# Optimization experiments

Hardware: AMD Instinct MI355X
Metric: run time of the kernel (lower is better)

Reference implementation:

```python
import jax, jax.numpy as jnp
import numpy as np

B, T, DIN, DM, NC = 8, 4096, 1024, 256, 157
DILS = (1, 2, 4, 8, 16)


def _conv1(w, x, b=None):
    # 1x1 conv: w [out,in], x [B,in,T] -> [B,out,T]
    y = jnp.einsum('oi,bit->bot', w, x)
    return y if b is None else y + b[None, :, None]


def _dal(x, wq, wk, wv, d):
    # Dilated 3-tap multiplicative local attention (DAL block, groups=1).
    # Taps in the zero-padded (pad=d) sequence at offsets 0, d, 2d == positions t-d, t, t+d.
    _, _, T_ = x.shape
    xp = jnp.pad(x, ((0, 0), (0, 0), (d, d)))
    q = _conv1(wq, x)                 # [B,C,T]
    kp = _conv1(wk, xp)               # [B,C,T+2d]
    vp = _conv1(wv, xp)
    k = jnp.stack([kp[:, :, 0:T_], kp[:, :, d:T_ + d], kp[:, :, 2 * d:T_ + 2 * d]], axis=-1)  # [B,C,T,3]
    v = jnp.stack([vp[:, :, 0:T_], vp[:, :, d:T_ + d], vp[:, :, 2 * d:T_ + 2 * d]], axis=-1)
    attn = jax.nn.softmax(q[..., None] * k, axis=-1)  # softmax over the 3 taps
    return jnp.sum(attn * v, axis=-1)  # [B,C,T]


def _fwd(x, mask, bottle0_w, bottle0_b,
         dal1_wq, dal1_wk, dal1_wv, bottle1_w, bottle1_b,
         dal2_wq, dal2_wk, dal2_wv, bottle2_w, bottle2_b,
         dal3_wq, dal3_wk, dal3_wv, bottle3_w, bottle3_b,
         dal4_wq, dal4_wk, dal4_wv, bottle4_w, bottle4_b,
         dal5_wq, dal5_wk, dal5_wv, bottle5_w, bottle5_b,
         bottle6_w, bottle6_b):
    m = mask[:, 0:1, :]
    out = _conv1(bottle0_w, x, bottle0_b)
    layers = [
        (dal1_wq, dal1_wk, dal1_wv, bottle1_w, bottle1_b),
        (dal2_wq, dal2_wk, dal2_wv, bottle2_w, bottle2_b),
        (dal3_wq, dal3_wk, dal3_wv, bottle3_w, bottle3_b),
        (dal4_wq, dal4_wk, dal4_wv, bottle4_w, bottle4_b),
        (dal5_wq, dal5_wk, dal5_wv, bottle5_w, bottle5_b),
    ]
    # Dropout layers are identity in eval mode.
    for (wq, wk, wv, bw, bb), d in zip(layers, DILS):
        h = jax.nn.relu(_dal(out, wq, wk, wv, d))
        h = _conv1(bw, h, bb)
        out = (out + h) * m
    return _conv1(bottle6_w, out, bottle6_b) * m  # [B,NC,T]


def setup_inputs() -> dict:
    key = jax.random.key(0)
    ks = jax.random.split(key, 32)
    s = 0.05
    inp = {}
    inp['x'] = jax.random.normal(ks[0], (B, DIN, T), jnp.float32)
    inp['mask'] = jnp.ones((B, 1, T), jnp.float32)
    inp['bottle0_w'] = jax.random.normal(ks[1], (DM, DIN), jnp.float32) * s
    inp['bottle0_b'] = jnp.zeros((DM,), jnp.float32)
    i = 2
    for l in range(1, 6):
        inp['dal%d_wq' % l] = jax.random.normal(ks[i], (DM, DM), jnp.float32) * s; i += 1
        inp['dal%d_wk' % l] = jax.random.normal(ks[i], (DM, DM), jnp.float32) * s; i += 1
        inp['dal%d_wv' % l] = jax.random.normal(ks[i], (DM, DM), jnp.float32) * s; i += 1
        inp['bottle%d_w' % l] = jax.random.normal(ks[i], (DM, DM), jnp.float32) * s; i += 1
        inp['bottle%d_b' % l] = jnp.zeros((DM,), jnp.float32)
    inp['bottle6_w'] = jax.random.normal(ks[i], (NC, DM), jnp.float32) * s
    inp['bottle6_b'] = jnp.zeros((NC,), jnp.float32)
    return inp


def reference(x, mask, bottle0_w, bottle0_b,
              dal1_wq, dal1_wk, dal1_wv, bottle1_w, bottle1_b,
              dal2_wq, dal2_wk, dal2_wv, bottle2_w, bottle2_b,
              dal3_wq, dal3_wk, dal3_wv, bottle3_w, bottle3_b,
              dal4_wq, dal4_wk, dal4_wv, bottle4_w, bottle4_b,
              dal5_wq, dal5_wk, dal5_wv, bottle5_w, bottle5_b,
              bottle6_w, bottle6_b):
    return _fwd(x, mask, bottle0_w, bottle0_b,
                dal1_wq, dal1_wk, dal1_wv, bottle1_w, bottle1_b,
                dal2_wq, dal2_wk, dal2_wv, bottle2_w, bottle2_b,
                dal3_wq, dal3_wk, dal3_wv, bottle3_w, bottle3_b,
                dal4_wq, dal4_wk, dal4_wv, bottle4_w, bottle4_b,
                dal5_wq, dal5_wk, dal5_wv, bottle5_w, bottle5_b,
                bottle6_w, bottle6_b)
```

## Files before the change

### kernel.cpp

```cpp
#include <hip/hip_runtime.h>
#include <hip/hip_bf16.h>
#include <stdint.h>

#define T_LEN 4096
#define B_SZ  8
#define D_IN  1024
#define D_M   256
#define N_C   157

typedef __attribute__((ext_vector_type(8))) short short8;
typedef __attribute__((ext_vector_type(4))) float floatx4;

static __device__ __forceinline__ unsigned short f2bf(float f) {
  unsigned u = __float_as_uint(f);
  u += 0x7FFFu + ((u >> 16) & 1u);
  return (unsigned short)(u >> 16);
}
static __device__ __forceinline__ float bf2f(unsigned short h) {
  return __uint_as_float(((unsigned)h) << 16);
}

static __device__ __forceinline__ void gl_lds16(const unsigned short* g,
                                                unsigned short* l) {
  __builtin_amdgcn_global_load_lds(
      (const __attribute__((address_space(1))) unsigned int*)g,
      (__attribute__((address_space(3))) unsigned int*)l, 16, 0, 0);
}

struct WSeg { const float* src; int n; int off; };
struct WPrepArgs { WSeg seg[22]; };

__global__ void wprep_kernel(WPrepArgs a, unsigned short* __restrict__ wbuf) {
  WSeg s = a.seg[blockIdx.x];
  for (int i = (blockIdx.y << 8) + threadIdx.x; i < s.n; i += (gridDim.y << 8))
    wbuf[s.off + i] = f2bf(s.src[i]);
}

__global__ void transpose_xT(const float* __restrict__ x,
                             unsigned short* __restrict__ xT) {
  __shared__ float tile[64][65];
  const int t0 = blockIdx.x << 6;
  const int i0 = blockIdx.y << 6;
  const int b  = blockIdx.z;
  const int tid = threadIdx.x;
  {
    const int row = tid >> 2;
    const int cc  = (tid & 3) << 4;
    const float* src = x + ((size_t)b * D_IN + (i0 + row)) * T_LEN + t0 + cc;
#pragma unroll
    for (int p = 0; p < 4; ++p) {
      float4 v = *(const float4*)(src + p * 4);
      tile[row][cc + p * 4 + 0] = v.x;
      tile[row][cc + p * 4 + 1] = v.y;
      tile[row][cc + p * 4 + 2] = v.z;
      tile[row][cc + p * 4 + 3] = v.w;
    }
  }
  __syncthreads();
#pragma unroll
  for (int it = 0; it < 2; ++it) {
    const int task = tid + (it << 8);
    const int tr = task >> 3;
    const int ic = (task & 7) << 3;
    short8 o;
#pragma unroll
    for (int j = 0; j < 8; ++j) o[j] = (short)f2bf(tile[ic + j][tr]);
    *(short8*)(xT + ((size_t)b * T_LEN + (t0 + tr)) * D_IN + i0 + ic) = o;
  }
}

template<bool ATTN, bool HAS_BIAS, bool HAS_RES, bool HAS_MASK,
         bool WRITE_BF16, bool SWAP_CT>
__global__ __launch_bounds__(256)
void gemm_kernel(const unsigned short* __restrict__ Xact,
                 const unsigned short* __restrict__ W,
                 const float* __restrict__ bias,
                 const unsigned short* __restrict__ residB,
                 const float* __restrict__ mask,
                 float* __restrict__ outF,
                 unsigned short* __restrict__ outB,
                 int K, int Mw, int dil) {
  __shared__ unsigned short sA[2][64 * 64];
  __shared__ unsigned short sB[2][128 * 64];

  const int bx = blockIdx.x;
  const int t0 = blockIdx.y << (SWAP_CT ? 7 : 6);
  const int b  = blockIdx.z;
  const int tid  = threadIdx.x;
  const int wv   = tid >> 6;
  const int lane = tid & 63;
  const int wn   = wv << 5;
  const int fm   = lane & 15;
  const int fq   = lane >> 4;
  const int lrow = lane >> 3;
  const int cbg8 = (((lane & 7) ^ lrow) << 3);

  const unsigned short* Xb =
      Xact + (size_t)b * T_LEN * (size_t)(ATTN ? 768 : K);
  const unsigned short* srcA =
      SWAP_CT ? (W + (size_t)(bx << 6) * K) : (Xb + (size_t)t0 * K);
  const unsigned short* srcB =
      SWAP_CT ? (Xb + (size_t)t0 * K) : (W + (size_t)(bx << 7) * K);

  const short8 z8 = {0, 0, 0, 0, 0, 0, 0, 0};
  const floatx4 fz = {0.f, 0.f, 0.f, 0.f};
  floatx4 acc[4][2];
#pragma unroll
  for (int i = 0; i < 4; ++i)
#pragma unroll
    for (int j = 0; j < 2; ++j) acc[i][j] = fz;

  auto stage = [&](int kk, int bufi) {
    if constexpr (ATTN) {
#pragma unroll
      for (int itp = 0; itp < 2; ++itp) {
        int c = tid + (itp << 8);
        int m = c >> 3;
        int cb = c & 7;
        int ch = kk + (cb << 3);
        int t = t0 + m;
        const unsigned short* base = Xb + (size_t)t * 768 + ch;
        short8 qv = *(const short8*)(base);
        short8 kc = *(const short8*)(base + 256);
        short8 vc = *(const short8*)(base + 512);
        short8 km = z8, kp = z8, vm = z8, vp = z8;
        const long off = (long)dil * 768;
        if (t >= dil) {
          km = *(const short8*)(base - off + 256);
          vm = *(const short8*)(base - off + 512);
        }
        if (t + dil < T_LEN) {
          kp = *(const short8*)(base + off + 256);
          vp = *(const short8*)(base + off + 512);
        }
        short8 o;
#pragma unroll
        for (int e = 0; e < 8; ++e) {
          float q  = bf2f((unsigned short)qv[e]);
          float s0 = q * bf2f((unsigned short)km[e]);
          float s1 = q * bf2f((unsigned short)kc[e]);
          float s2 = q * bf2f((unsigned short)kp[e]);
          float mx = fmaxf(s0, fmaxf(s1, s2));
          float e0 = __expf(s0 - mx), e1 = __expf(s1 - mx), e2 = __expf(s2 - mx);
          float num = e0 * bf2f((unsigned short)vm[e]) +
                      e1 * bf2f((unsigned short)vc[e]) +
                      e2 * bf2f((unsigned short)vp[e]);
          float r = num / (e0 + e1 + e2);
          o[e] = (short)f2bf(fmaxf(r, 0.0f));
        }
        *(short8*)&sA[bufi][(m << 6) + ((cb ^ (m & 7)) << 3)] = o;
      }
    } else {
#pragma unroll
      for (int p = 0; p < 2; ++p) {
        const int slot = (p << 2) + wv;
        gl_lds16(srcA + (size_t)((slot << 3) + lrow) * K + kk + cbg8,
                 &sA[bufi][slot * 512]);
      }
    }
#pragma unroll
    for (int p = 0; p < 4; ++p) {
      const int slot = (p << 2) + wv;
      gl_lds16(srcB + (size_t)((slot << 3) + lrow) * K + kk + cbg8,
               &sB[bufi][slot * 512]);
    }
  };

  const int niter = K >> 6;
  stage(0, 0);
  for (int it = 0; it < niter; ++it) {
    const int p = it & 1;
    __syncthreads();
    if (it + 1 < niter) stage((it + 1) << 6, 1 - p);
#pragma unroll
    for (int ks = 0; ks < 64; ks += 32) {
      const int cbase = ((fq + (ks >> 3)) ^ (fm & 7)) << 3;
      short8 af[4], bfr[2];
#pragma unroll
      for (int i = 0; i < 4; ++i)
        af[i] = *(short8*)&sA[p][(((i << 4) + fm) << 6) + cbase];
#pragma unroll
      for (int j = 0; j < 2; ++j)
        bfr[j] = *(short8*)&sB[p][((wn + (j << 4) + fm) << 6) + cbase];
#pragma unroll
      for (int i = 0; i < 4; ++i)
#pragma unroll
        for (int j = 0; j < 2; ++j)
          acc[i][j] = __builtin_amdgcn_mfma_f32_16x16x32_bf16(
              af[i], bfr[j], acc[i][j], 0, 0, 0);
    }
  }

  if constexpr (SWAP_CT) {
#pragma unroll
    for (int i = 0; i < 4; ++i) {
#pragma unroll
      for (int r = 0; r < 4; ++r) {
        const int o = (bx << 6) + (i << 4) + (fq << 2) + r;
        if (o >= Mw) continue;
        const float bi = HAS_BIAS ? bias[o] : 0.0f;
#pragma unroll
        for (int j = 0; j < 2; ++j) {
          const int t = t0 + wn + (j << 4) + fm;
          float val = acc[i][j][r] + bi;
          if (HAS_MASK) val *= mask[(size_t)b * T_LEN + t];
          outF[((size_t)b * Mw + o) * T_LEN + t] = val;
        }
      }
    }
  } else {
#pragma unroll
    for (int i = 0; i < 4; ++i) {
#pragma unroll
      for (int j = 0; j < 2; ++j) {
        const int co = (bx << 7) + wn + (j << 4) + fm;
        if (co >= Mw) continue;
        const float bi = HAS_BIAS ? bias[co] : 0.0f;
#pragma unroll
        for (int r = 0; r < 4; ++r) {
          const int t = t0 + (i << 4) + (fq << 2) + r;
          float val = acc[i][j][r] + bi;
          const size_t idx = ((size_t)b * T_LEN + t) * (size_t)Mw + co;
          if (HAS_RES) val += bf2f(residB[idx]);
          if (HAS_MASK) val *= mask[(size_t)b * T_LEN + t];
          if (WRITE_BF16) outB[idx] = f2bf(val);
        }
      }
    }
  }
}

extern "C" void kernel_launch(void* const* d_in, const int* in_sizes, int n_in,
                              void* d_out, int out_size, void* d_ws, size_t ws_size,
                              hipStream_t stream) {
  const float* x    = (const float*)d_in[0];
  const float* mask = (const float*)d_in[1];

  char* ws = (char*)d_ws;
  unsigned short* xT   = (unsigned short*)ws;
  unsigned short* qkv  = xT;
  unsigned short* outB = (unsigned short*)(ws + 67108864);
  unsigned short* wbuf = (unsigned short*)(ws + 83886080);

  const int WB0  = 0;
  const int WQKV = 262144;
  const int WBT  = 1245184;
  const int WB6  = 1572864;

  WPrepArgs pa;
  int si = 0;
  pa.seg[si++] = { (const float*)d_in[2], 262144, WB0 };
  for (int l = 0; l < 5; ++l) {
    int bi = 4 + l * 5;
    pa.seg[si++] = { (const float*)d_in[bi + 0], 65536, WQKV + l * 196608 };
    pa.seg[si++] = { (const float*)d_in[bi + 1], 65536, WQKV + l * 196608 + 65536 };
    pa.seg[si++] = { (const float*)d_in[bi + 2], 65536, WQKV + l * 196608 + 131072 };
    pa.seg[si++] = { (const float*)d_in[bi + 3], 65536, WBT + l * 65536 };
  }
  pa.seg[si++] = { (const float*)d_in[29], 40192, WB6 };

  wprep_kernel<<<dim3(22, 64), 256, 0, stream>>>(pa, wbuf);
  transpose_xT<<<dim3(64, 16, 8), 256, 0, stream>>>(x, xT);

  gemm_kernel<false, true, false, false, true, false>
      <<<dim3(2, 64, 8), 256, 0, stream>>>(
          xT, wbuf + WB0, (const float*)d_in[3], nullptr, mask,
          nullptr, outB, 1024, 256, 0);

  const int dils[5] = {1, 2, 4, 8, 16};
  for (int l = 0; l < 5; ++l) {
    int bi = 4 + l * 5;
    gemm_kernel<false, false, false, false, true, false>
        <<<dim3(6, 64, 8), 256, 0, stream>>>(
            outB, wbuf + WQKV + l * 196608, nullptr, nullptr, mask,
            nullptr, qkv, 256, 768, 0);
    gemm_kernel<true, true, true, true, true, false>
        <<<dim3(2, 64, 8), 256, 0, stream>>>(
            qkv, wbuf + WBT + l * 65536, (const float*)d_in[bi + 4], outB, mask,
            nullptr, outB, 256, 256, dils[l]);
  }

  gemm_kernel<false, true, false, true, false, true>
      <<<dim3(3, 32, 8), 256, 0, stream>>>(
          outB, wbuf + WB6, (const float*)d_in[30], nullptr, mask,
          (float*)d_out, nullptr, 256, 157, 0);
}
```

Before: 653.5 us.

## Fuse QKV projection, dilated attention and bottleneck GEMM into one layer kernel

Result: no change. 660.7 us (+1.1%).

```diff
diff --git a/kernel.cpp b/kernel.cpp
--- a/kernel.cpp
+++ b/kernel.cpp
@@ -69,17 +69,15 @@
   }
 }
 
-template<bool ATTN, bool HAS_BIAS, bool HAS_RES, bool HAS_MASK,
-         bool WRITE_BF16, bool SWAP_CT>
+template<bool HAS_BIAS, bool HAS_MASK, bool SWAP_CT>
 __global__ __launch_bounds__(256)
 void gemm_kernel(const unsigned short* __restrict__ Xact,
                  const unsigned short* __restrict__ W,
                  const float* __restrict__ bias,
-                 const unsigned short* __restrict__ residB,
                  const float* __restrict__ mask,
                  float* __restrict__ outF,
                  unsigned short* __restrict__ outB,
-                 int K, int Mw, int dil) {
+                 int K, int Mw) {
   __shared__ unsigned short sA[2][64 * 64];
   __shared__ unsigned short sB[2][128 * 64];
 
@@ -95,14 +93,12 @@
   const int lrow = lane >> 3;
   const int cbg8 = (((lane & 7) ^ lrow) << 3);
 
-  const unsigned short* Xb =
-      Xact + (size_t)b * T_LEN * (size_t)(ATTN ? 768 : K);
+  const unsigned short* Xb = Xact + (size_t)b * T_LEN * (size_t)K;
   const unsigned short* srcA =
       SWAP_CT ? (W + (size_t)(bx << 6) * K) : (Xb + (size_t)t0 * K);
   const unsigned short* srcB =
       SWAP_CT ? (Xb + (size_t)t0 * K) : (W + (size_t)(bx << 7) * K);
 
-  const short8 z8 = {0, 0, 0, 0, 0, 0, 0, 0};
   const floatx4 fz = {0.f, 0.f, 0.f, 0.f};
   floatx4 acc[4][2];
 #pragma unroll
@@ -111,52 +107,11 @@
     for (int j = 0; j < 2; ++j) acc[i][j] = fz;
 
   auto stage = [&](int kk, int bufi) {
-    if constexpr (ATTN) {
-#pragma unroll
-      for (int itp = 0; itp < 2; ++itp) {
-        int c = tid + (itp << 8);
-        int m = c >> 3;
-        int cb = c & 7;
-        int ch = kk + (cb << 3);
-        int t = t0 + m;
-        const unsigned short* base = Xb + (size_t)t * 768 + ch;
-        short8 qv = *(const short8*)(base);
-        short8 kc = *(const short8*)(base + 256);
-        short8 vc = *(const short8*)(base + 512);
-        short8 km = z8, kp = z8, vm = z8, vp = z8;
-        const long off = (long)dil * 768;
-        if (t >= dil) {
-          km = *(const short8*)(base - off + 256);
-          vm = *(const short8*)(base - off + 512);
-        }
-        if (t + dil < T_LEN) {
-          kp = *(const short8*)(base + off + 256);
-          vp = *(const short8*)(base + off + 512);
-        }
-        short8 o;
-#pragma unroll
-        for (int e = 0; e < 8; ++e) {
-          float q  = bf2f((unsigned short)qv[e]);
-          float s0 = q * bf2f((unsigned short)km[e]);
-          float s1 = q * bf2f((unsigned short)kc[e]);
-          float s2 = q * bf2f((unsigned short)kp[e]);
-          float mx = fmaxf(s0, fmaxf(s1, s2));
-          float e0 = __expf(s0 - mx), e1 = __expf(s1 - mx), e2 = __expf(s2 - mx);
-          float num = e0 * bf2f((unsigned short)vm[e]) +
-                      e1 * bf2f((unsigned short)vc[e]) +
-                      e2 * bf2f((unsigned short)vp[e]);
-          float r = num / (e0 + e1 + e2);
-          o[e] = (short)f2bf(fmaxf(r, 0.0f));
-        }
-        *(short8*)&sA[bufi][(m << 6) + ((cb ^ (m & 7)) << 3)] = o;
-      }
-    } else {
-#pragma unroll
-      for (int p = 0; p < 2; ++p) {
-        const int slot = (p << 2) + wv;
-        gl_lds16(srcA + (size_t)((slot << 3) + lrow) * K + kk + cbg8,
-                 &sA[bufi][slot * 512]);
-      }
+#pragma unroll
+    for (int p = 0; p < 2; ++p) {
+      const int slot = (p << 2) + wv;
+      gl_lds16(srcA + (size_t)((slot << 3) + lrow) * K + kk + cbg8,
+               &sA[bufi][slot * 512]);
     }
 #pragma unroll
     for (int p = 0; p < 4; ++p) {
@@ -220,14 +175,220 @@
         for (int r = 0; r < 4; ++r) {
           const int t = t0 + (i << 4) + (fq << 2) + r;
           float val = acc[i][j][r] + bi;
-          const size_t idx = ((size_t)b * T_LEN + t) * (size_t)Mw + co;
-          if (HAS_RES) val += bf2f(residB[idx]);
           if (HAS_MASK) val *= mask[(size_t)b * T_LEN + t];
-          if (WRITE_BF16) outB[idx] = f2bf(val);
+          outB[((size_t)b * T_LEN + t) * (size_t)Mw + co] = f2bf(val);
         }
       }
     }
   }
+}
+
+__global__ __launch_bounds__(256)
+void layer_kernel(const unsigned short* __restrict__ outPrev,
+                  const unsigned short* __restrict__ Wall,
+                  const unsigned short* __restrict__ Wb,
+                  const float* __restrict__ bias,
+                  const float* __restrict__ mask,
+                  unsigned short* __restrict__ outNext,
+                  int dil) {
+  __shared__ unsigned short lds[70400];
+  unsigned short* xh    = lds;
+  unsigned short* hbuf  = lds + 24576;
+  unsigned short* chunk = lds + 41472;
+  unsigned short* wst   = lds + 62208;
+
+  const int t0 = blockIdx.x << 6;
+  const int b  = blockIdx.y;
+  const int tid  = threadIdx.x;
+  const int wv   = tid >> 6;
+  const int lane = tid & 63;
+  const int fm   = lane & 15;
+  const int fq   = lane >> 4;
+  const int wh   = wv >> 1;
+  const int nh   = wv & 1;
+
+  const unsigned short* src = outPrev + (size_t)b * T_LEN * 256;
+
+#pragma unroll
+  for (int p = 0; p < 12; ++p) {
+    const int slot = (p << 2) + wv;
+    const int row  = (slot << 1) + (lane >> 5);
+    int t = t0 - 16 + row;
+    t = t < 0 ? 0 : (t >= T_LEN ? T_LEN - 1 : t);
+    const int kb = (lane & 31) ^ (row & 7);
+    gl_lds16(src + (size_t)t * 256 + (kb << 3), xh + (slot << 9));
+  }
+  __syncthreads();
+  if (t0 == 0) {
+    *(short8*)&xh[tid << 4] = short8{0,0,0,0,0,0,0,0};
+    *(short8*)&xh[(tid << 4) + 8] = short8{0,0,0,0,0,0,0,0};
+  }
+  if (t0 == T_LEN - 64) {
+    *(short8*)&xh[20480 + (tid << 4)] = short8{0,0,0,0,0,0,0,0};
+    *(short8*)&xh[20480 + (tid << 4) + 8] = short8{0,0,0,0,0,0,0,0};
+  }
+  __syncthreads();
+
+#pragma unroll 1
+  for (int j = 0; j < 4; ++j) {
+#pragma unroll 1
+    for (int sec = 0; sec < 3; ++sec) {
+      const unsigned short* Wsec = Wall + (size_t)((sec << 8) + (j << 6)) * 256;
+#pragma unroll
+      for (int p = 0; p < 2; ++p) {
+        const int slot = (p << 2) + wv;
+        const int rw = (slot << 3) + (lane >> 3);
+        const int kb = (lane & 7) ^ (lane >> 3);
+        gl_lds16(Wsec + (size_t)rw * 256 + (kb << 3), wst + (slot << 9));
+      }
+      floatx4 accB[3][2];
+#pragma unroll
+      for (int i = 0; i < 3; ++i)
+#pragma unroll
+        for (int jj = 0; jj < 2; ++jj) accB[i][jj] = floatx4{0.f,0.f,0.f,0.f};
+
+      for (int kt = 0; kt < 4; ++kt) {
+        __syncthreads();
+        if (kt < 3) {
+          const int nb = (kt + 1) & 1;
+#pragma unroll
+          for (int p = 0; p < 2; ++p) {
+            const int slot = (p << 2) + wv;
+            const int rw = (slot << 3) + (lane >> 3);
+            const int kb = (lane & 7) ^ (lane >> 3);
+            gl_lds16(Wsec + (size_t)rw * 256 + ((kt + 1) << 6) + (kb << 3),
+                     wst + (nb << 12) + (slot << 9));
+          }
+        }
+        const unsigned short* wb = wst + ((kt & 1) << 12);
+#pragma unroll
+        for (int ks = 0; ks < 64; ks += 32) {
+          short8 af[3], bfr[2];
+#pragma unroll
+          for (int i = 0; i < 3; ++i) {
+            const int row = 48 * wh + (i << 4) + fm;
+            const int cb = ((kt << 3) + (ks >> 3) + fq) ^ (fm & 7);
+            af[i] = *(short8*)&xh[(row << 8) + (cb << 3)];
+          }
+#pragma unroll
+          for (int jj = 0; jj < 2; ++jj) {
+            const int nr = (nh << 5) + (jj << 4) + fm;
+            const int cb = ((ks >> 3) + fq) ^ (fm & 7);
+            bfr[jj] = *(short8*)&wb[(nr << 6) + (cb << 3)];
+          }
+#pragma unroll
+          for (int i = 0; i < 3; ++i)
+#pragma unroll
+            for (int jj = 0; jj < 2; ++jj)
+              accB[i][jj] = __builtin_amdgcn_mfma_f32_16x16x32_bf16(
+                  af[i], bfr[jj], accB[i][jj], 0, 0, 0);
+        }
+      }
+#pragma unroll
+      for (int i = 0; i < 3; ++i)
+#pragma unroll
+        for (int jj = 0; jj < 2; ++jj)
+#pragma unroll
+          for (int r = 0; r < 4; ++r) {
+            const int row = 48 * wh + (i << 4) + (fq << 2) + r;
+            const int col = (nh << 5) + (jj << 4) + fm;
+            chunk[sec * 6912 + row * 72 + col] = f2bf(accB[i][jj][r]);
+          }
+    }
+    __syncthreads();
+#pragma unroll
+    for (int p = 0; p < 2; ++p) {
+      const int task = (p << 8) + tid;
+      const int tr = task >> 3;
+      const int c8 = (task & 7) << 3;
+      const int rq = (16 + tr) * 72 + c8;
+      short8 qv = *(short8*)&chunk[rq];
+      short8 kc = *(short8*)&chunk[6912 + rq];
+      short8 vc = *(short8*)&chunk[13824 + rq];
+      short8 km = *(short8*)&chunk[6912 + (16 + tr - dil) * 72 + c8];
+      short8 kp = *(short8*)&chunk[6912 + (16 + tr + dil) * 72 + c8];
+      short8 vm = *(short8*)&chunk[13824 + (16 + tr - dil) * 72 + c8];
+      short8 vp = *(short8*)&chunk[13824 + (16 + tr + dil) * 72 + c8];
+      short8 o;
+#pragma unroll
+      for (int e = 0; e < 8; ++e) {
+        float q  = bf2f((unsigned short)qv[e]);
+        float s0 = q * bf2f((unsigned short)km[e]);
+        float s1 = q * bf2f((unsigned short)kc[e]);
+        float s2 = q * bf2f((unsigned short)kp[e]);
+        float mx = fmaxf(s0, fmaxf(s1, s2));
+        float e0 = __expf(s0 - mx), e1 = __expf(s1 - mx), e2 = __expf(s2 - mx);
+        float num = e0 * bf2f((unsigned short)vm[e]) +
+                    e1 * bf2f((unsigned short)vc[e]) +
+                    e2 * bf2f((unsigned short)vp[e]);
+        float r = num / (e0 + e1 + e2);
+        o[e] = (short)f2bf(fmaxf(r, 0.0f));
+      }
+      *(short8*)&hbuf[tr * 264 + (j << 6) + c8] = o;
+    }
+    __syncthreads();
+  }
+
+  floatx4 accC[4][4];
+#pragma unroll
+  for (int i = 0; i < 4; ++i)
+#pragma unroll
+    for (int jj = 0; jj < 4; ++jj) accC[i][jj] = floatx4{0.f,0.f,0.f,0.f};
+
+#pragma unroll
+  for (int p = 0; p < 4; ++p) {
+    const int slot = (p << 2) + wv;
+    const int rw = (slot << 4) + (lane >> 2);
+    gl_lds16(Wb + (size_t)rw * 256 + ((lane & 3) << 3), chunk + (slot << 9));
+  }
+  for (int kt = 0; kt < 8; ++kt) {
+    __syncthreads();
+    if (kt < 7) {
+      const int nb = (kt + 1) & 1;
+#pragma unroll
+      for (int p = 0; p < 4; ++p) {
+        const int slot = (p << 2) + wv;
+        const int rw = (slot << 4) + (lane >> 2);
+        gl_lds16(Wb + (size_t)rw * 256 + ((kt + 1) << 5) + ((lane & 3) << 3),
+                 chunk + (nb << 13) + (slot << 9));
+      }
+    }
+    const unsigned short* cbuf = chunk + ((kt & 1) << 13);
+    short8 af[4], bfr[4];
+#pragma unroll
+    for (int i = 0; i < 4; ++i) {
+      const int row = (i << 4) + fm;
+      af[i] = *(short8*)&hbuf[row * 264 + (kt << 5) + (fq << 3)];
+    }
+#pragma unroll
+    for (int jj = 0; jj < 4; ++jj) {
+      const int nr = (wv << 6) + (jj << 4) + fm;
+      bfr[jj] = *(short8*)&cbuf[(nr << 5) + (fq << 3)];
+    }
+#pragma unroll
+    for (int i = 0; i < 4; ++i)
+#pragma unroll
+      for (int jj = 0; jj < 4; ++jj)
+        accC[i][jj] = __builtin_amdgcn_mfma_f32_16x16x32_bf16(
+            af[i], bfr[jj], accC[i][jj], 0, 0, 0);
+  }
+
+#pragma unroll
+  for (int i = 0; i < 4; ++i)
+#pragma unroll
+    for (int jj = 0; jj < 4; ++jj) {
+      const int co = (wv << 6) + (jj << 4) + fm;
+      const float bi = bias[co];
+#pragma unroll
+      for (int r = 0; r < 4; ++r) {
+        const int tl = (i << 4) + (fq << 2) + r;
+        const int xr = 16 + tl;
+        float val = accC[i][jj][r] + bi;
+        val += bf2f(xh[(xr << 8) + ((((co >> 3)) ^ (xr & 7)) << 3) + (co & 7)]);
+        val *= mask[(size_t)b * T_LEN + t0 + tl];
+        outNext[((size_t)b * T_LEN + t0 + tl) * 256 + co] = f2bf(val);
+      }
+    }
 }
 
 extern "C" void kernel_launch(void* const* d_in, const int* in_sizes, int n_in,
@@ -238,9 +399,9 @@
 
   char* ws = (char*)d_ws;
   unsigned short* xT   = (unsigned short*)ws;
-  unsigned short* qkv  = xT;
-  unsigned short* outB = (unsigned short*)(ws + 67108864);
-  unsigned short* wbuf = (unsigned short*)(ws + 83886080);
+  unsigned short* out0 = (unsigned short*)(ws + 67108864);
+  unsigned short* out1 = (unsigned short*)(ws + 83886080);
+  unsigned short* wbuf = (unsigned short*)(ws + 100663296);
 
   const int WB0  = 0;
   const int WQKV = 262144;
@@ -262,26 +423,21 @@
   wprep_kernel<<<dim3(22, 64), 256, 0, stream>>>(pa, wbuf);
   transpose_xT<<<dim3(64, 16, 8), 256, 0, stream>>>(x, xT);
 
-  gemm_kernel<false, true, false, false, true, false>
+  gemm_kernel<true, false, false>
       <<<dim3(2, 64, 8), 256, 0, stream>>>(
-          xT, wbuf + WB0, (const float*)d_in[3], nullptr, mask,
-          nullptr, outB, 1024, 256, 0);
+          xT, wbuf + WB0, (const float*)d_in[3], mask, nullptr, out0, 1024, 256);
 
   const int dils[5] = {1, 2, 4, 8, 16};
+  unsigned short* pp[2] = { out0, out1 };
   for (int l = 0; l < 5; ++l) {
     int bi = 4 + l * 5;
-    gemm_kernel<false, false, false, false, true, false>
-        <<<dim3(6, 64, 8), 256, 0, stream>>>(
-            outB, wbuf + WQKV + l * 196608, nullptr, nullptr, mask,
-            nullptr, qkv, 256, 768, 0);
-    gemm_kernel<true, true, true, true, true, false>
-        <<<dim3(2, 64, 8), 256, 0, stream>>>(
-            qkv, wbuf + WBT + l * 65536, (const float*)d_in[bi + 4], outB, mask,
-            nullptr, outB, 256, 256, dils[l]);
-  }
-
-  gemm_kernel<false, true, false, true, false, true>
+    layer_kernel<<<dim3(64, 8), 256, 0, stream>>>(
+        pp[l & 1], wbuf + WQKV + l * 196608, wbuf + WBT + l * 65536,
+        (const float*)d_in[bi + 4], mask, pp[(l + 1) & 1], dils[l]);
+  }
+
+  gemm_kernel<true, true, true>
       <<<dim3(3, 32, 8), 256, 0, stream>>>(
-          outB, wbuf + WB6, (const float*)d_in[30], nullptr, mask,
-          (float*)d_out, nullptr, 256, 157, 0);
-}
+          pp[1], wbuf + WB6, (const float*)d_in[30], mask,
+          (float*)d_out, nullptr, 256, 157);
+}
```
